# Kernel tuning notes

Measured on AMD Instinct MI355X. Metric: run time of the kernel, lower is better.

## Reference

```python
import jax, jax.numpy as jnp
import numpy as np

LAM = 5.0
NUM_STEPS = 100
B, N, D = 8, 1024, 256


def setup_inputs() -> dict:
    key = jax.random.key(0)
    k1, k2 = jax.random.split(key)
    fA = jax.random.normal(k1, (B, N, D), dtype=jnp.float32)
    fB = jax.random.normal(k2, (B, N, D), dtype=jnp.float32)
    dustbin = jnp.zeros((1,), dtype=jnp.float32)  # learned dustbin score, init 0.0
    return {"fA": fA, "fB": fB, "dustbin": dustbin}


def _l2_normalize(x, eps=1e-12):
    # matches tf.math.l2_normalize: x / sqrt(max(sum(x^2), eps))
    return x * jax.lax.rsqrt(jnp.maximum(jnp.sum(x * x, axis=-1, keepdims=True), eps))


def _forward(fA, fB, dustbin):
    b, n, _ = fA.shape
    fA = _l2_normalize(fA)
    fB = _l2_normalize(fB)
    Sij = jnp.einsum('bnd,bmd->bnm', fA, fB)  # (B, N, N)
    # augment with dustbin row/col -> (B, N+1, N+1)
    row = dustbin * jnp.ones((b, 1, n), Sij.dtype)
    col = dustbin * jnp.ones((b, n + 1, 1), Sij.dtype)
    S_aug = jnp.concatenate([jnp.concatenate([Sij, row], axis=1), col], axis=2)
    Cij = jnp.clip(-S_aug, -15.0 / LAM, 15.0 / LAM)
    # marginals: [1,...,1, N] for both rows and cols
    ab = jnp.concatenate([jnp.ones((n,), Sij.dtype), jnp.full((1,), float(n), Sij.dtype)])[None, :]  # (1, N+1)
    P = jnp.exp(-LAM * Cij)
    P = P / jnp.sum(P, axis=(1, 2), keepdims=True)

    def step(P, _):
        # NOTE: row_sum/col_sum both computed from the SAME P, as in the TF code
        row_sum = jnp.sum(P, axis=1)  # (B, N+1)
        col_sum = jnp.sum(P, axis=2)  # (B, N+1)
        P = P * (ab / col_sum)[:, :, None]
        P = P * (ab / row_sum)[:, None, :]
        return P, None

    P, _ = jax.lax.scan(jax.checkpoint(step), P, None, length=NUM_STEPS)
    return P


def reference(fA, fB, dustbin):
    return _forward(fA, fB, dustbin)
```

## Files before the change

kernel.cpp:

```cpp
#include <hip/hip_runtime.h>
#include <math.h>
#include <stdint.h>

#define NB 8
#define NN 1024
#define DD 256
#define NP1 1025
#define NSTEPS 100

__global__ __launch_bounds__(256) void norm_kernel(const float* __restrict__ fA,
                                                   const float* __restrict__ fB,
                                                   float* __restrict__ invA,
                                                   float* __restrict__ invB) {
  int gw = (blockIdx.x * 256 + threadIdx.x) >> 6;
  int lane = threadIdx.x & 63;
  const float* src;
  float* dst;
  int row;
  if (gw < NB * NN) { src = fA; dst = invA; row = gw; }
  else              { src = fB; dst = invB; row = gw - NB * NN; }
  float4 v = *(const float4*)(src + (size_t)row * DD + lane * 4);
  double ss = (double)v.x * v.x + (double)v.y * v.y + (double)v.z * v.z + (double)v.w * v.w;
#pragma unroll
  for (int o = 32; o; o >>= 1) ss += __shfl_xor(ss, o, 64);
  if (lane == 0) dst[row] = (float)(1.0 / sqrt(fmax(ss, 1e-12)));
}

__global__ __launch_bounds__(256) void gemm_exp_kernel(const float* __restrict__ fA,
                                                       const float* __restrict__ fB,
                                                       const float* __restrict__ invA,
                                                       const float* __restrict__ invB,
                                                       float* __restrict__ P0,
                                                       double* __restrict__ partZ) {
  const int id = blockIdx.x;
  const int b = id & 7;
  const int tile = id >> 3;
  const int bx = tile & 15, by = tile >> 4;
  const int row0 = by * 64, col0 = bx * 64;
  const int tid = threadIdx.x;
  const int tx = tid & 15, ty = tid >> 4;
  __shared__ __align__(16) float As[16][68];
  __shared__ __align__(16) float Bs[16][68];
  __shared__ __align__(16) float Ts[64][68];
  __shared__ double zred[256];
  float acc[4][4] = {{0.f}};
  const int lm = tid >> 2, kq = (tid & 3) << 2;
  const float sa = invA[b * NN + row0 + lm];
  const float sb = invB[b * NN + col0 + lm];
  const float* pA = fA + (size_t)(b * NN + row0 + lm) * DD + kq;
  const float* pB = fB + (size_t)(b * NN + col0 + lm) * DD + kq;
  for (int k0 = 0; k0 < DD; k0 += 16) {
    const float4 a4 = *(const float4*)(pA + k0);
    const float4 b4 = *(const float4*)(pB + k0);
    As[kq + 0][lm] = a4.x * sa; As[kq + 1][lm] = a4.y * sa;
    As[kq + 2][lm] = a4.z * sa; As[kq + 3][lm] = a4.w * sa;
    Bs[kq + 0][lm] = b4.x * sb; Bs[kq + 1][lm] = b4.y * sb;
    Bs[kq + 2][lm] = b4.z * sb; Bs[kq + 3][lm] = b4.w * sb;
    __syncthreads();
#pragma unroll
    for (int kk = 0; kk < 16; ++kk) {
      const float4 av = *(const float4*)&As[kk][ty * 4];
      const float4 bv = *(const float4*)&Bs[kk][tx * 4];
      const float ar[4] = {av.x, av.y, av.z, av.w};
      const float br[4] = {bv.x, bv.y, bv.z, bv.w};
#pragma unroll
      for (int a = 0; a < 4; ++a)
#pragma unroll
        for (int e = 0; e < 4; ++e)
          acc[a][e] = fmaf(ar[a], br[e], acc[a][e]);
    }
    __syncthreads();
  }
  double zs = 0.0;
#pragma unroll
  for (int a = 0; a < 4; ++a)
#pragma unroll
    for (int e = 0; e < 4; ++e) {
      const float S = acc[a][e];
      const float C = fminf(fmaxf(-S, -3.0f), 3.0f);
      const float p = expf(-5.0f * C);
      acc[a][e] = p;
      zs += (double)p;
    }
  zred[tid] = zs;
  __syncthreads();
#pragma unroll
  for (int o = 128; o; o >>= 1) {
    if (tid < o) zred[tid] += zred[tid + o];
    __syncthreads();
  }
  if (tid == 0) partZ[(b * 16 + by) * 16 + bx] = zred[0];
#pragma unroll
  for (int a = 0; a < 4; ++a)
#pragma unroll
    for (int e = 0; e < 4; ++e)
      Ts[ty * 4 + a][tx * 4 + e] = acc[a][e];
  __syncthreads();
  {
    const int lane = tid & 63, w = tid >> 6;
    float* P0b = P0 + (size_t)b * NP1 * NP1;
    for (int j = w; j < 64; j += 4)
      P0b[(size_t)(row0 + j) * NP1 + col0 + lane] = Ts[j][lane];
  }
}

__global__ __launch_bounds__(1024) void fill_dustbin_kernel(const float* __restrict__ dustbin,
                                                            float* __restrict__ P0) {
  const int b = blockIdx.x, tid = threadIdx.x;
  const float d = dustbin[0];
  const float dv = expf(-5.0f * fminf(fmaxf(-d, -3.0f), 3.0f));
  float* P0b = P0 + (size_t)b * NP1 * NP1;
  for (int j = tid; j < NP1; j += 1024) {
    P0b[(size_t)NN * NP1 + j] = dv;
    P0b[(size_t)j * NP1 + NN] = dv;
  }
}

__global__ __launch_bounds__(256) void init_rc_kernel(const double* __restrict__ partZ,
                                                      float* __restrict__ r0,
                                                      double* __restrict__ Binit,
                                                      double* __restrict__ Bzero) {
  const int b = blockIdx.x, tid = threadIdx.x;
  __shared__ double red[256];
  red[tid] = partZ[b * 256 + tid];
  __syncthreads();
#pragma unroll
  for (int o = 128; o; o >>= 1) {
    if (tid < o) red[tid] += red[tid + o];
    __syncthreads();
  }
  const double Z = red[0];
  const float rv = (float)(1.0 / Z);
  for (int i = tid; i < NP1; i += 256) {
    r0[b * NP1 + i] = rv;
    Binit[b * NP1 + i] = (i == NN) ? (double)NN : 1.0;
    Bzero[b * NP1 + i] = 0.0;
  }
}

__global__ __launch_bounds__(512) void step_kernel(const float* __restrict__ P0,
                                                   const float* __restrict__ rin,
                                                   float* __restrict__ rout,
                                                   const double* __restrict__ Bprev,
                                                   double* __restrict__ Bacc,
                                                   double* __restrict__ Bzero) {
  const int id = blockIdx.x;
  const int b = id & 7;
  const int s = id >> 3;
  const int tid = threadIdx.x;
  const int lane = tid & 63;
  const int wv = tid >> 6;

  __shared__ float c_lds[NP1];
  __shared__ float part_lds[8][NP1];

  {
    const int base = id * 16;
    if (tid < 16) {
      const int idx = base + tid;
      if (idx < NB * NP1) Bzero[idx] = 0.0;
    }
  }
  const double* Bp = Bprev + b * NP1;
  for (int j = tid; j < NP1; j += 512) {
    const double ab = (j == NN) ? (double)NN : 1.0;
    c_lds[j] = (float)(ab / Bp[j]);
  }
  __syncthreads();

  const float* P0b = P0 + (size_t)b * NP1 * NP1;
  const float* rv_in = rin + b * NP1;
  const int rowA = s * 16 + wv;
  const int rowB = rowA + 8;
  const bool vA = rowA < NP1;
  const bool vB = rowB < NP1;
  const int rA = vA ? rowA : NN;
  const int rB = vB ? rowB : NN;
  const float wA = vA ? rv_in[rowA] : 0.0f;
  const float wB = vB ? rv_in[rowB] : 0.0f;
  const float* pA = P0b + (size_t)rA * NP1;
  const float* pB = P0b + (size_t)rB * NP1;

  double dotA = 0.0, dotB = 0.0;
  float part[16];
#pragma unroll
  for (int k = 0; k < 16; ++k) part[k] = 0.0f;

  float stA[16], stB[16];
#pragma unroll
  for (int k = 0; k < 16; ++k) {
    const int j = lane + (k << 6);
    stA[k] = pA[j];
    stB[k] = pB[j];
  }
#pragma unroll
  for (int k = 0; k < 16; ++k) {
    const int j = lane + (k << 6);
    const double cj = (double)c_lds[j];
    dotA += (double)stA[k] * cj;
    dotB += (double)stB[k] * cj;
    part[k] = fmaf(wA, stA[k], fmaf(wB, stB[k], part[k]));
  }
  float ptail = 0.0f;
  if (lane == 0) {
    const float aT = pA[NN], bT = pB[NN];
    const double cN = (double)c_lds[NN];
    dotA += (double)aT * cN;
    dotB += (double)bT * cN;
    ptail = wA * aT + wB * bT;
  }
#pragma unroll
  for (int o = 32; o; o >>= 1) {
    dotA += __shfl_xor(dotA, o, 64);
    dotB += __shfl_xor(dotB, o, 64);
  }
  if (lane == 0) {
    float* ro = rout + b * NP1;
    if (vA) ro[rowA] = (float)((rowA == NN ? (double)NN : 1.0) / dotA);
    if (vB) ro[rowB] = (float)((rowB == NN ? (double)NN : 1.0) / dotB);
  }
#pragma unroll
  for (int k = 0; k < 16; ++k) part_lds[wv][lane + (k << 6)] = part[k];
  if (lane == 0) part_lds[wv][NN] = ptail;
  __syncthreads();
  double* Ba = Bacc + b * NP1;
  for (int j = tid; j < NP1; j += 512) {
    const float s0 = ((part_lds[0][j] + part_lds[1][j]) + (part_lds[2][j] + part_lds[3][j])) +
                     ((part_lds[4][j] + part_lds[5][j]) + (part_lds[6][j] + part_lds[7][j]));
    atomicAdd(Ba + j, (double)s0);
  }
}

__global__ __launch_bounds__(256) void cfinal_kernel(const double* __restrict__ Bfin,
                                                     float* __restrict__ cfin) {
  const int b = blockIdx.x;
  for (int j = threadIdx.x; j < NP1; j += 256)
    cfin[b * NP1 + j] = (float)(((j == NN) ? (double)NN : 1.0) / Bfin[b * NP1 + j]);
}

__global__ __launch_bounds__(256) void finalize_kernel(float* __restrict__ P,
                                                       const float* __restrict__ rfin,
                                                       const float* __restrict__ cfin) {
  const int bi = blockIdx.x;
  const int b = bi & 7, i = bi >> 3;
  const float rv = rfin[b * NP1 + i];
  float* row = P + (size_t)b * NP1 * NP1 + (size_t)i * NP1;
  const float* cv = cfin + b * NP1;
  for (int j = threadIdx.x; j < NP1; j += 256) row[j] = rv * row[j] * cv[j];
}

extern "C" void kernel_launch(void* const* d_in, const int* in_sizes, int n_in,
                              void* d_out, int out_size, void* d_ws, size_t ws_size,
                              hipStream_t stream) {
  const float* fA = (const float*)d_in[0];
  const float* fB = (const float*)d_in[1];
  const float* dustbin = (const float*)d_in[2];

  float* P0 = (float*)d_out;

  float* rbuf = (float*)d_ws;
  float* cfin = rbuf + 2 * NB * NP1;
  double* Bbuf = (double*)(((uintptr_t)(cfin + NB * NP1) + 15) & ~(uintptr_t)15);
  double* partZ = Bbuf + 3 * NB * NP1;
  float* invA = (float*)(partZ + NB * 256);
  float* invB = invA + NB * NN;

  norm_kernel<<<4096, 256, 0, stream>>>(fA, fB, invA, invB);
  gemm_exp_kernel<<<2048, 256, 0, stream>>>(fA, fB, invA, invB, P0, partZ);
  fill_dustbin_kernel<<<NB, 1024, 0, stream>>>(dustbin, P0);
  init_rc_kernel<<<NB, 256, 0, stream>>>(partZ, rbuf, Bbuf + 2 * NB * NP1, Bbuf);

  for (int t = 0; t < NSTEPS; ++t) {
    float* rin = rbuf + (t & 1) * NB * NP1;
    float* rout = rbuf + ((t + 1) & 1) * NB * NP1;
    double* Bprev = Bbuf + ((t + 2) % 3) * NB * NP1;
    double* Bacc = Bbuf + (t % 3) * NB * NP1;
    double* Bzero = Bbuf + ((t + 1) % 3) * NB * NP1;
    step_kernel<<<520, 512, 0, stream>>>(P0, rin, rout, Bprev, Bacc, Bzero);
  }

  cfinal_kernel<<<NB, 256, 0, stream>>>(Bbuf, cfin);
  finalize_kernel<<<NB * NP1, 256, 0, stream>>>(P0, rbuf, cfin);
}
```

Baseline: 1.009 ms.

## Pad P0 rows to 1028 floats in workspace and vectorize step loads

Moves the unnormalized matrix P0 into workspace with a padded row stride of 1028 floats, so rows are 16-byte aligned and can be read with float4 loads in the step, GEMM epilogue and finalize kernels. The GEMM writes its output directly as float4 instead of staging it through shared memory. The dustbin row is folded into the last block, which cuts the step grid from 520 to 512 blocks and removes the per-row validity checks. Column scales are kept in double in LDS and an occupancy hint is added. In exchange, finalize must write into the unpadded output, and more workspace is used.

```diff
diff --git a/kernel.cpp b/kernel.cpp
--- a/kernel.cpp
+++ b/kernel.cpp
@@ -6,6 +6,7 @@
 #define NN 1024
 #define DD 256
 #define NP1 1025
+#define LDP 1028
 #define NSTEPS 100
 
 __global__ __launch_bounds__(256) void norm_kernel(const float* __restrict__ fA,
@@ -41,7 +42,6 @@
   const int tx = tid & 15, ty = tid >> 4;
   __shared__ __align__(16) float As[16][68];
   __shared__ __align__(16) float Bs[16][68];
-  __shared__ __align__(16) float Ts[64][68];
   __shared__ double zred[256];
   float acc[4][4] = {{0.f}};
   const int lm = tid >> 2, kq = (tid & 3) << 2;
@@ -82,6 +82,15 @@
       acc[a][e] = p;
       zs += (double)p;
     }
+  {
+    float* P0b = P0 + (size_t)b * NP1 * LDP;
+#pragma unroll
+    for (int a = 0; a < 4; ++a) {
+      float4 v;
+      v.x = acc[a][0]; v.y = acc[a][1]; v.z = acc[a][2]; v.w = acc[a][3];
+      *(float4*)(P0b + (size_t)(row0 + ty * 4 + a) * LDP + col0 + tx * 4) = v;
+    }
+  }
   zred[tid] = zs;
   __syncthreads();
 #pragma unroll
@@ -90,18 +99,6 @@
     __syncthreads();
   }
   if (tid == 0) partZ[(b * 16 + by) * 16 + bx] = zred[0];
-#pragma unroll
-  for (int a = 0; a < 4; ++a)
-#pragma unroll
-    for (int e = 0; e < 4; ++e)
-      Ts[ty * 4 + a][tx * 4 + e] = acc[a][e];
-  __syncthreads();
-  {
-    const int lane = tid & 63, w = tid >> 6;
-    float* P0b = P0 + (size_t)b * NP1 * NP1;
-    for (int j = w; j < 64; j += 4)
-      P0b[(size_t)(row0 + j) * NP1 + col0 + lane] = Ts[j][lane];
-  }
 }
 
 __global__ __launch_bounds__(1024) void fill_dustbin_kernel(const float* __restrict__ dustbin,
@@ -109,10 +106,10 @@
   const int b = blockIdx.x, tid = threadIdx.x;
   const float d = dustbin[0];
   const float dv = expf(-5.0f * fminf(fmaxf(-d, -3.0f), 3.0f));
-  float* P0b = P0 + (size_t)b * NP1 * NP1;
+  float* P0b = P0 + (size_t)b * NP1 * LDP;
   for (int j = tid; j < NP1; j += 1024) {
-    P0b[(size_t)NN * NP1 + j] = dv;
-    P0b[(size_t)j * NP1 + NN] = dv;
+    P0b[(size_t)NN * LDP + j] = dv;
+    P0b[(size_t)j * LDP + NN] = dv;
   }
 }
 
@@ -138,12 +135,12 @@
   }
 }
 
-__global__ __launch_bounds__(512) void step_kernel(const float* __restrict__ P0,
-                                                   const float* __restrict__ rin,
-                                                   float* __restrict__ rout,
-                                                   const double* __restrict__ Bprev,
-                                                   double* __restrict__ Bacc,
-                                                   double* __restrict__ Bzero) {
+__global__ __launch_bounds__(512, 4) void step_kernel(const float* __restrict__ P0,
+                                                      const float* __restrict__ rin,
+                                                      float* __restrict__ rout,
+                                                      const double* __restrict__ Bprev,
+                                                      double* __restrict__ Bacc,
+                                                      double* __restrict__ Bzero) {
   const int id = blockIdx.x;
   const int b = id & 7;
   const int s = id >> 3;
@@ -151,77 +148,102 @@
   const int lane = tid & 63;
   const int wv = tid >> 6;
 
-  __shared__ float c_lds[NP1];
-  __shared__ float part_lds[8][NP1];
-
-  {
-    const int base = id * 16;
-    if (tid < 16) {
-      const int idx = base + tid;
-      if (idx < NB * NP1) Bzero[idx] = 0.0;
-    }
-  }
-  const double* Bp = Bprev + b * NP1;
-  for (int j = tid; j < NP1; j += 512) {
-    const double ab = (j == NN) ? (double)NN : 1.0;
-    c_lds[j] = (float)(ab / Bp[j]);
-  }
-  __syncthreads();
-
-  const float* P0b = P0 + (size_t)b * NP1 * NP1;
+  __shared__ __align__(16) double c_lds[NP1 + 3];
+  __shared__ __align__(16) float part_lds[8][LDP];
+
+  const float* P0b = P0 + (size_t)b * NP1 * LDP;
   const float* rv_in = rin + b * NP1;
   const int rowA = s * 16 + wv;
   const int rowB = rowA + 8;
-  const bool vA = rowA < NP1;
-  const bool vB = rowB < NP1;
-  const int rA = vA ? rowA : NN;
-  const int rB = vB ? rowB : NN;
-  const float wA = vA ? rv_in[rowA] : 0.0f;
-  const float wB = vB ? rv_in[rowB] : 0.0f;
-  const float* pA = P0b + (size_t)rA * NP1;
-  const float* pB = P0b + (size_t)rB * NP1;
-
-  double dotA = 0.0, dotB = 0.0;
-  float part[16];
-#pragma unroll
-  for (int k = 0; k < 16; ++k) part[k] = 0.0f;
-
-  float stA[16], stB[16];
-#pragma unroll
-  for (int k = 0; k < 16; ++k) {
-    const int j = lane + (k << 6);
-    stA[k] = pA[j];
-    stB[k] = pB[j];
-  }
-#pragma unroll
-  for (int k = 0; k < 16; ++k) {
-    const int j = lane + (k << 6);
-    const double cj = (double)c_lds[j];
-    dotA += (double)stA[k] * cj;
-    dotB += (double)stB[k] * cj;
-    part[k] = fmaf(wA, stA[k], fmaf(wB, stB[k], part[k]));
-  }
-  float ptail = 0.0f;
+  const bool special = (s == 63 && wv == 7);
+  const float wA = rv_in[rowA];
+  const float wB = rv_in[rowB];
+  const float4* pA4 = (const float4*)(P0b + (size_t)rowA * LDP);
+  const float4* pB4 = (const float4*)(P0b + (size_t)rowB * LDP);
+  const float4* pC4 = (const float4*)(P0b + (size_t)NN * LDP);
+
+  float4 a4[4], b4[4];
+#pragma unroll
+  for (int k = 0; k < 4; ++k) {
+    a4[k] = pA4[lane + (k << 6)];
+    b4[k] = pB4[lane + (k << 6)];
+  }
+  float aT = 0.f, bT = 0.f;
   if (lane == 0) {
-    const float aT = pA[NN], bT = pB[NN];
-    const double cN = (double)c_lds[NN];
+    aT = ((const float*)pA4)[NN];
+    bT = ((const float*)pB4)[NN];
+  }
+  float4 c4[4];
+  float cT = 0.f, wC = 0.f;
+  if (special) {
+#pragma unroll
+    for (int k = 0; k < 4; ++k) c4[k] = pC4[lane + (k << 6)];
+    if (lane == 0) cT = ((const float*)pC4)[NN];
+    wC = rv_in[NN];
+  }
+
+  if (tid < 17) {
+    const int idx = id * 17 + tid;
+    if (idx < NB * NP1) Bzero[idx] = 0.0;
+  }
+  const double* Bp = Bprev + b * NP1;
+  for (int j = tid; j < NP1; j += 512)
+    c_lds[j] = ((j == NN) ? (double)NN : 1.0) / Bp[j];
+  __syncthreads();
+
+  double dotA = 0.0, dotB = 0.0, dotC = 0.0;
+  float4 part[4];
+#pragma unroll
+  for (int k = 0; k < 4; ++k) {
+    const int j4 = lane + (k << 6);
+    const double2 c01 = *(const double2*)&c_lds[4 * j4];
+    const double2 c23 = *(const double2*)&c_lds[4 * j4 + 2];
+    dotA += (double)a4[k].x * c01.x + (double)a4[k].y * c01.y +
+            (double)a4[k].z * c23.x + (double)a4[k].w * c23.y;
+    dotB += (double)b4[k].x * c01.x + (double)b4[k].y * c01.y +
+            (double)b4[k].z * c23.x + (double)b4[k].w * c23.y;
+    part[k].x = fmaf(wA, a4[k].x, wB * b4[k].x);
+    part[k].y = fmaf(wA, a4[k].y, wB * b4[k].y);
+    part[k].z = fmaf(wA, a4[k].z, wB * b4[k].z);
+    part[k].w = fmaf(wA, a4[k].w, wB * b4[k].w);
+    if (special) {
+      dotC += (double)c4[k].x * c01.x + (double)c4[k].y * c01.y +
+              (double)c4[k].z * c23.x + (double)c4[k].w * c23.y;
+      part[k].x = fmaf(wC, c4[k].x, part[k].x);
+      part[k].y = fmaf(wC, c4[k].y, part[k].y);
+      part[k].z = fmaf(wC, c4[k].z, part[k].z);
+      part[k].w = fmaf(wC, c4[k].w, part[k].w);
+    }
+  }
+  float ptail = 0.f;
+  if (lane == 0) {
+    const double cN = c_lds[NN];
     dotA += (double)aT * cN;
     dotB += (double)bT * cN;
     ptail = wA * aT + wB * bT;
+    if (special) { dotC += (double)cT * cN; ptail = fmaf(wC, cT, ptail); }
   }
 #pragma unroll
   for (int o = 32; o; o >>= 1) {
     dotA += __shfl_xor(dotA, o, 64);
     dotB += __shfl_xor(dotB, o, 64);
   }
+  if (special) {
+#pragma unroll
+    for (int o = 32; o; o >>= 1) dotC += __shfl_xor(dotC, o, 64);
+  }
   if (lane == 0) {
     float* ro = rout + b * NP1;
-    if (vA) ro[rowA] = (float)((rowA == NN ? (double)NN : 1.0) / dotA);
-    if (vB) ro[rowB] = (float)((rowB == NN ? (double)NN : 1.0) / dotB);
-  }
-#pragma unroll
-  for (int k = 0; k < 16; ++k) part_lds[wv][lane + (k << 6)] = part[k];
-  if (lane == 0) part_lds[wv][NN] = ptail;
+    ro[rowA] = (float)(1.0 / dotA);
+    ro[rowB] = (float)(1.0 / dotB);
+    if (special) ro[NN] = (float)((double)NN / dotC);
+  }
+  {
+    float4* pl4 = (float4*)&part_lds[wv][0];
+#pragma unroll
+    for (int k = 0; k < 4; ++k) pl4[lane + (k << 6)] = part[k];
+    if (lane == 0) part_lds[wv][NN] = ptail;
+  }
   __syncthreads();
   double* Ba = Bacc + b * NP1;
   for (int j = tid; j < NP1; j += 512) {
@@ -235,18 +257,28 @@
                                                      float* __restrict__ cfin) {
   const int b = blockIdx.x;
   for (int j = threadIdx.x; j < NP1; j += 256)
-    cfin[b * NP1 + j] = (float)(((j == NN) ? (double)NN : 1.0) / Bfin[b * NP1 + j]);
-}
-
-__global__ __launch_bounds__(256) void finalize_kernel(float* __restrict__ P,
+    cfin[b * LDP + j] = (float)(((j == NN) ? (double)NN : 1.0) / Bfin[b * NP1 + j]);
+}
+
+__global__ __launch_bounds__(256) void finalize_kernel(const float* __restrict__ P0,
+                                                       float* __restrict__ Pout,
                                                        const float* __restrict__ rfin,
                                                        const float* __restrict__ cfin) {
   const int bi = blockIdx.x;
   const int b = bi & 7, i = bi >> 3;
+  const int tid = threadIdx.x;
   const float rv = rfin[b * NP1 + i];
-  float* row = P + (size_t)b * NP1 * NP1 + (size_t)i * NP1;
-  const float* cv = cfin + b * NP1;
-  for (int j = threadIdx.x; j < NP1; j += 256) row[j] = rv * row[j] * cv[j];
+  const float4* src = (const float4*)(P0 + (size_t)b * NP1 * LDP + (size_t)i * LDP);
+  const float4* cv = (const float4*)(cfin + b * LDP);
+  float* dst = Pout + (size_t)b * NP1 * NP1 + (size_t)i * NP1;
+  const float4 p = src[tid];
+  const float4 c = cv[tid];
+  dst[tid * 4 + 0] = rv * p.x * c.x;
+  dst[tid * 4 + 1] = rv * p.y * c.y;
+  dst[tid * 4 + 2] = rv * p.z * c.z;
+  dst[tid * 4 + 3] = rv * p.w * c.w;
+  if (tid == 0)
+    dst[NN] = rv * ((const float*)src)[NN] * cfin[b * LDP + NN];
 }
 
 extern "C" void kernel_launch(void* const* d_in, const int* in_sizes, int n_in,
@@ -256,11 +288,12 @@
   const float* fB = (const float*)d_in[1];
   const float* dustbin = (const float*)d_in[2];
 
-  float* P0 = (float*)d_out;
-
-  float* rbuf = (float*)d_ws;
+  float* Pout = (float*)d_out;
+
+  float* P0 = (float*)d_ws;
+  float* rbuf = P0 + (size_t)NB * NP1 * LDP;
   float* cfin = rbuf + 2 * NB * NP1;
-  double* Bbuf = (double*)(((uintptr_t)(cfin + NB * NP1) + 15) & ~(uintptr_t)15);
+  double* Bbuf = (double*)(((uintptr_t)(cfin + NB * LDP) + 15) & ~(uintptr_t)15);
   double* partZ = Bbuf + 3 * NB * NP1;
   float* invA = (float*)(partZ + NB * 256);
   float* invB = invA + NB * NN;
@@ -276,9 +309,9 @@
     double* Bprev = Bbuf + ((t + 2) % 3) * NB * NP1;
     double* Bacc = Bbuf + (t % 3) * NB * NP1;
     double* Bzero = Bbuf + ((t + 1) % 3) * NB * NP1;
-    step_kernel<<<520, 512, 0, stream>>>(P0, rin, rout, Bprev, Bacc, Bzero);
+    step_kernel<<<512, 512, 0, stream>>>(P0, rin, rout, Bprev, Bacc, Bzero);
   }
 
   cfinal_kernel<<<NB, 256, 0, stream>>>(Bbuf, cfin);
-  finalize_kernel<<<NB * NP1, 256, 0, stream>>>(P0, rbuf, cfin);
-}
+  finalize_kernel<<<NB * NP1, 256, 0, stream>>>(P0, Pout, rbuf, cfin);
+}
```

Measured after the change: 967.6 us. 1.04x faster.
